# Performance work log

Measured on AMD Instinct MI355X. Metric: run time of the kernel, lower is better.

## Reference

```python
import jax, jax.numpy as jnp
import numpy as np

N, B, D = 2048, 2, 512
H, R = 8, 3
C = D // H  # head dim = 64


def setup_inputs() -> dict:
    key = jax.random.key(0)
    ks = jax.random.split(key, 12)
    x_q = jax.random.normal(ks[0], (N, B, D), jnp.float32)
    x_k = jax.random.normal(ks[1], (N, B, D), jnp.float32)
    x_v = jax.random.normal(ks[2], (N, B, D), jnp.float32)
    attn_mask = jax.random.randint(ks[3], (B, R, N, N), 0, 2).astype(bool)
    # pad the last 128 key positions (realistic padding; avoids all -inf rows)
    key_padding_mask = jnp.zeros((B, N), bool).at[:, -128:].set(True)
    s = 1.0 / np.sqrt(D)
    Wq = jax.random.normal(ks[4], (D, D), jnp.float32) * s
    Wk = jax.random.normal(ks[5], (D, D), jnp.float32) * s
    Wv = jax.random.normal(ks[6], (D, D), jnp.float32) * s
    Wo = jax.random.normal(ks[7], (D, D), jnp.float32) * s
    bq = jnp.zeros((D,), jnp.float32)
    bk = jnp.zeros((D,), jnp.float32)
    bv = jnp.zeros((D,), jnp.float32)
    bo = jnp.zeros((D,), jnp.float32)
    # mask_weight: randn, last column set to sqrt(head_dim) as in __init__
    mask_weight = jax.random.normal(ks[8], (H, R + 1), jnp.float32)
    mask_weight = mask_weight.at[:, -1].set(np.sqrt(C))
    return dict(x_q=x_q, x_k=x_k, x_v=x_v, attn_mask=attn_mask,
                key_padding_mask=key_padding_mask, Wq=Wq, bq=bq, Wk=Wk, bk=bk,
                Wv=Wv, bv=bv, Wo=Wo, bo=bo, mask_weight=mask_weight)


def _split_heads(x):
    # (n, b, h*c) -> (b, h, n, c)
    n, b, _ = x.shape
    return jnp.transpose(x.reshape(n, b, H, C), (1, 2, 0, 3))


def reference(x_q, x_k, x_v, attn_mask, key_padding_mask,
              Wq, bq, Wk, bk, Wv, bv, Wo, bo, mask_weight):
    q = _split_heads(x_q @ Wq + bq)  # (b,h,n,c)
    k = _split_heads(x_k @ Wk + bk)
    v = _split_heads(x_v @ Wv + bv)

    # relative bias: softmax over edge-type weights, scaled per head
    rel_w = jax.nn.softmax(mask_weight[:, :-1], axis=-1)  # (h,r)
    inv_mask = (~attn_mask).astype(jnp.float32)           # (b,r,n,m)
    rel = jnp.einsum('hr,h,brnm->bhnm', rel_w, mask_weight[:, -1], inv_mask)
    rel = jnp.where(key_padding_mask[:, None, None, :], -jnp.inf, rel)

    # scaled dot-product attention (torch default scale = 1/sqrt(head_dim))
    scores = jnp.einsum('bhnc,bhmc->bhnm', q, k) * (1.0 / np.sqrt(C))
    attn = jax.nn.softmax(scores + rel, axis=-1)
    o = jnp.einsum('bhnm,bhmc->bhnc', attn, v)

    # (b,h,n,c) -> (n,b,h*c)
    n = o.shape[2]
    o = jnp.transpose(o, (2, 0, 1, 3)).reshape(n, o.shape[0], H * C)
    return o @ Wo + bo
```

## Files before the change

### kernel.cpp

```cpp
#include <hip/hip_runtime.h>
#include <hip/hip_bf16.h>

#define NN 2048
#define LOG2E 1.4426950408889634f

typedef unsigned int u32;
typedef unsigned short u16;
typedef unsigned char u8;

typedef __attribute__((ext_vector_type(8))) short short8;
typedef __attribute__((ext_vector_type(4))) float f32x4;

__device__ __forceinline__ u16 f2bf(float f){
  __hip_bfloat16 h = __float2bfloat16(f);
  return *reinterpret_cast<u16*>(&h);
}
__device__ __forceinline__ u32 pack2(float a, float b){
  return (u32)f2bf(a) | ((u32)f2bf(b) << 16);
}
__device__ __forceinline__ void gload16(const void* g, void* l){
  __builtin_amdgcn_global_load_lds((const __attribute__((address_space(1))) u32*)g,
                                   (__attribute__((address_space(3))) u32*)l, 16, 0, 0);
}

__global__ __launch_bounds__(256)
void prep_k(const int* __restrict__ am, const int* __restrict__ kp,
            u8* __restrict__ cmb)
{
  const size_t tid  = (size_t)blockIdx.x * 256 + threadIdx.x;
  const size_t base = tid * 4;
  const int row = (int)(base >> 11);
  const int m0  = (int)(base & 2047);
  const int b = row >> 11, n = row & 2047;
  const size_t e0 = (((size_t)(b*3) * NN) + n) * NN + m0;
  const int4 a0 = *reinterpret_cast<const int4*>(am + e0);
  const int4 a1 = *reinterpret_cast<const int4*>(am + e0 + (size_t)NN*NN);
  const int4 a2 = *reinterpret_cast<const int4*>(am + e0 + 2*(size_t)NN*NN);
  const int4 kv = *reinterpret_cast<const int4*>(kp + (size_t)b*NN + m0);
  const int a0v[4] = {a0.x,a0.y,a0.z,a0.w};
  const int a1v[4] = {a1.x,a1.y,a1.z,a1.w};
  const int a2v[4] = {a2.x,a2.y,a2.z,a2.w};
  const int kvv[4] = {kv.x,kv.y,kv.z,kv.w};
  uchar4 out;
  u8* o = (u8*)&out;
  #pragma unroll
  for (int i = 0; i < 4; ++i)
    o[i] = (u8)((a0v[i]?1:0) | (a1v[i]?2:0) | (a2v[i]?4:0) | (kvv[i]?8:0));
  *reinterpret_cast<uchar4*>(cmb + base) = out;
}

__global__ __launch_bounds__(256)
void trw3_k(const float* __restrict__ W0, const float* __restrict__ W1,
            const float* __restrict__ W2, u16* __restrict__ WT)
{
  __shared__ float tile[32][33];
  const float* W = (blockIdx.z == 0) ? W0 : (blockIdx.z == 1) ? W1 : W2;
  u16* dst = WT + (size_t)blockIdx.z * 262144;
  const int t = threadIdx.x;
  const int k0 = blockIdx.x * 32, n0 = blockIdx.y * 32;
  const int c = t & 31, r = t >> 5;
  #pragma unroll
  for (int i = 0; i < 4; ++i)
    tile[r + 8*i][c] = W[(size_t)(k0 + r + 8*i) * 512 + n0 + c];
  __syncthreads();
  #pragma unroll
  for (int i = 0; i < 4; ++i)
    dst[(size_t)(n0 + r + 8*i) * 512 + k0 + c] = f2bf(tile[c][r + 8*i]);
}

__global__ __launch_bounds__(256)
void trw_k(const float* __restrict__ W, u16* __restrict__ WT)
{
  __shared__ float tile[32][33];
  const int t = threadIdx.x;
  const int k0 = blockIdx.x * 32, n0 = blockIdx.y * 32;
  const int c = t & 31, r = t >> 5;
  #pragma unroll
  for (int i = 0; i < 4; ++i)
    tile[r + 8*i][c] = W[(size_t)(k0 + r + 8*i) * 512 + n0 + c];
  __syncthreads();
  #pragma unroll
  for (int i = 0; i < 4; ++i)
    WT[(size_t)(n0 + r + 8*i) * 512 + k0 + c] = f2bf(tile[c][r + 8*i]);
}

template<int BN, bool SCATTER, bool ABF16, bool OUTF32>
__device__ __forceinline__
void gemm_core(const void* __restrict__ Av, const u16* __restrict__ WT,
               const float* __restrict__ bias, void* __restrict__ Cd,
               float scale, int m0, int n0)
{
  constexpr int NI  = BN / 64;
  constexpr int WNL = BN / 32;
  __shared__ u16 As[2][64*64];
  __shared__ u16 Ws[2][BN*64];

  const int t = threadIdx.x;
  const int lane = t & 63;
  const int w = t >> 6;
  const int g = lane >> 4, r15 = lane & 15;
  const int wn = w * (BN/4);

  const int arow = t >> 2, akc = (t & 3) * 16, as0 = (t & 3) * 2;
  const int wrn = (BN==128) ? (t>>1) : (t>>2);
  const int wkc = (BN==128) ? ((t&1)*32) : ((t&3)*16);
  const int wsb = (BN==128) ? ((t&1)*4)  : ((t&3)*2);

  uint4  war[WNL];
  uint4  aab[2];
  float4 aaf[4];

  auto loadA = [&](int k0){
    if constexpr (ABF16) {
      const u16* A = (const u16*)Av;
      aab[0] = *reinterpret_cast<const uint4*>(A + (size_t)(m0+arow)*512 + k0 + akc);
      aab[1] = *reinterpret_cast<const uint4*>(A + (size_t)(m0+arow)*512 + k0 + akc + 8);
    } else {
      const float* A = (const float*)Av;
      #pragma unroll
      for (int q = 0; q < 4; ++q)
        aaf[q] = *reinterpret_cast<const float4*>(A + (size_t)(m0+arow)*512 + k0 + akc + 4*q);
    }
  };
  auto loadW = [&](int k0){
    #pragma unroll
    for (int i = 0; i < WNL; ++i)
      war[i] = *reinterpret_cast<const uint4*>(WT + (size_t)(n0+wrn)*512 + k0 + wkc + 8*i);
  };
  auto writeA = [&](int bf){
    uint4 v0, v1;
    if constexpr (ABF16) { v0 = aab[0]; v1 = aab[1]; }
    else {
      v0.x = pack2(aaf[0].x, aaf[0].y); v0.y = pack2(aaf[0].z, aaf[0].w);
      v0.z = pack2(aaf[1].x, aaf[1].y); v0.w = pack2(aaf[1].z, aaf[1].w);
      v1.x = pack2(aaf[2].x, aaf[2].y); v1.y = pack2(aaf[2].z, aaf[2].w);
      v1.z = pack2(aaf[3].x, aaf[3].y); v1.w = pack2(aaf[3].z, aaf[3].w);
    }
    *reinterpret_cast<uint4*>(&As[bf][arow*64 + (((as0  ) ^ (arow&7)) << 3)]) = v0;
    *reinterpret_cast<uint4*>(&As[bf][arow*64 + (((as0+1) ^ (arow&7)) << 3)]) = v1;
  };
  auto writeW = [&](int bf){
    #pragma unroll
    for (int i = 0; i < WNL; ++i)
      *reinterpret_cast<uint4*>(&Ws[bf][wrn*64 + (((wsb+i) ^ (wrn&7)) << 3)]) = war[i];
  };

  const f32x4 fz = {0.f,0.f,0.f,0.f};
  f32x4 acc[4][NI];
  #pragma unroll
  for (int mi = 0; mi < 4; ++mi)
    #pragma unroll
    for (int ni = 0; ni < NI; ++ni) acc[mi][ni] = fz;

  loadA(0); loadW(0);
  writeA(0); writeW(0);
  __syncthreads();

  for (int kt = 0; kt < 8; ++kt) {
    const int cur = kt & 1;
    if (kt < 7) { loadA((kt+1)*64); loadW((kt+1)*64); }
    #pragma unroll
    for (int ks = 0; ks < 2; ++ks) {
      short8 bfr[NI], afr[4];
      #pragma unroll
      for (int ni = 0; ni < NI; ++ni) {
        const int n = wn + 16*ni + r15;
        bfr[ni] = *reinterpret_cast<const short8*>(&Ws[cur][n*64 + (((ks*4+g) ^ (n&7)) << 3)]);
      }
      #pragma unroll
      for (int mi = 0; mi < 4; ++mi) {
        const int m = 16*mi + r15;
        afr[mi] = *reinterpret_cast<const short8*>(&As[cur][m*64 + (((ks*4+g) ^ (m&7)) << 3)]);
      }
      #pragma unroll
      for (int mi = 0; mi < 4; ++mi)
        #pragma unroll
        for (int ni = 0; ni < NI; ++ni)
          acc[mi][ni] = __builtin_amdgcn_mfma_f32_16x16x32_bf16(afr[mi], bfr[ni], acc[mi][ni], 0, 0, 0);
    }
    if (kt < 7) { writeA(cur^1); writeW(cur^1); }
    __syncthreads();
  }

  float bia[NI];
  #pragma unroll
  for (int ni = 0; ni < NI; ++ni) bia[ni] = bias[n0 + wn + 16*ni + r15];
  #pragma unroll
  for (int mi = 0; mi < 4; ++mi) {
    #pragma unroll
    for (int ni = 0; ni < NI; ++ni) {
      #pragma unroll
      for (int j = 0; j < 4; ++j) {
        const int row = m0 + 16*mi + 4*g + j;
        const int col = n0 + wn + 16*ni + r15;
        const float v = (acc[mi][ni][j] + bia[ni]) * scale;
        if constexpr (SCATTER) {
          const int bb = row & 1, ntok = row >> 1;
          const int h = col >> 6, c = col & 63;
          ((u16*)Cd)[(((size_t)(bb*8 + h) * NN + ntok) * 64) + c] = f2bf(v);
        } else if constexpr (OUTF32) {
          ((float*)Cd)[(size_t)row * 512 + col] = v;
        } else {
          ((u16*)Cd)[(size_t)row * 512 + col] = f2bf(v);
        }
      }
    }
  }
}

__global__ __launch_bounds__(256)
void gemm_qkv(const float* __restrict__ x0, const float* __restrict__ x1,
              const float* __restrict__ x2, const u16* __restrict__ WT3,
              const float* __restrict__ b0, const float* __restrict__ b1,
              const float* __restrict__ b2, u16* __restrict__ dst, float qscale)
{
  const int z = blockIdx.z;
  const float* A    = (z == 0) ? x0 : (z == 1) ? x1 : x2;
  const float* bias = (z == 0) ? b0 : (z == 1) ? b1 : b2;
  gemm_core<128, true, false, false>(A, WT3 + (size_t)z*262144, bias,
                                     dst + (size_t)z*2097152,
                                     (z == 0) ? qscale : 1.0f,
                                     blockIdx.x*64, blockIdx.y*128);
}

__global__ __launch_bounds__(256)
void gemm_wo(const u16* __restrict__ Ob, const u16* __restrict__ WT,
             const float* __restrict__ bias, float* __restrict__ out)
{
  gemm_core<64, false, true, true>(Ob, WT, bias, out, 1.0f,
                                   blockIdx.x*64, blockIdx.y*64);
}

__global__ __launch_bounds__(512)
void attn_mfma(const u16* __restrict__ Q, const u16* __restrict__ K,
               const u16* __restrict__ V, const u8* __restrict__ cmb,
               const float* __restrict__ mw, u16* __restrict__ O,
               float* __restrict__ Opart, float2* __restrict__ Ml, int kspan)
{
  __shared__ u16 Ks[2][64*64];
  __shared__ u16 Vs[2][64*64];
  __shared__ float lut[16];

  const int t = threadIdx.x;
  const int lane = t & 63;
  const int w = t >> 6;
  const int g = lane >> 4;
  const int r15 = lane & 15;
  const int bh = blockIdx.y;
  const int z = blockIdx.z;
  const int b = bh >> 3, h = bh & 7;
  const int n0 = blockIdx.x * 128;
  const int nq = n0 + w*16 + r15;
  const int k_beg = z * kspan;
  const float NEGINF = -__builtin_inff();

  if (t < 16) {
    const float mw0 = mw[h*4+0], mw1 = mw[h*4+1], mw2 = mw[h*4+2];
    const float msc = mw[h*4+3];
    const float mxw = fmaxf(mw0, fmaxf(mw1, mw2));
    const float e0 = __expf(mw0-mxw), e1 = __expf(mw1-mxw), e2 = __expf(mw2-mxw);
    const float inv = msc / (e0+e1+e2);
    float v = ((t & 1) ? 0.f : e0*inv) + ((t & 2) ? 0.f : e1*inv)
            + ((t & 4) ? 0.f : e2*inv);
    lut[t] = (t & 8) ? NEGINF : v * LOG2E;
  }

  const u16* qrow = Q + ((size_t)bh*NN + nq)*64;
  const short8 bq0 = *reinterpret_cast<const short8*>(qrow + 8*g);
  const short8 bq1 = *reinterpret_cast<const short8*>(qrow + 32 + 8*g);

  const u8* crow = cmb + ((size_t)(b*NN + nq))*NN;
  const u16* Kbase = K + (size_t)bh*NN*64;
  const u16* Vbase = V + (size_t)bh*NN*64;

  float m_run = NEGINF, l_run = 0.f;
  const f32x4 fz = {0.f, 0.f, 0.f, 0.f};
  f32x4 oacc[4] = {fz, fz, fz, fz};

  const int sm  = t >> 3;
  const int ssl = t & 7;
  const int kcol = (ssl ^ (sm & 7)) * 8;
  const int sc0 = (t & 7) * 8;
  const int aA = (((g & 1) << 5) + r15) << 2;
  const int aB = aA + 64;

  uint4 vreg;
  auto gloadK = [&](int m0, int bf){
    gload16(Kbase + (size_t)(m0 + sm)*64 + kcol, &Ks[bf][w*512 + (lane << 3)]);
  };
  auto loadV = [&](int m0){
    vreg = *reinterpret_cast<const uint4*>(Vbase + (size_t)(m0 + sm)*64 + sc0);
  };
  auto writeV = [&](int bf){
    u16 e[8];
    e[0]=vreg.x&0xffff; e[1]=vreg.x>>16; e[2]=vreg.y&0xffff; e[3]=vreg.y>>16;
    e[4]=vreg.z&0xffff; e[5]=vreg.z>>16; e[6]=vreg.w&0xffff; e[7]=vreg.w>>16;
    #pragma unroll
    for (int i = 0; i < 8; ++i) {
      const int c = sc0 + i;
      Vs[bf][c*64 + ((((sm>>3) ^ (c&7) ^ (c>>3)) << 3) | (sm & 7))] = e[i];
    }
  };

  const int ntiles = kspan >> 6;
  gloadK(k_beg, 0);
  loadV(k_beg);
  writeV(0);
  __syncthreads();

  for (int it = 0; it < ntiles; ++it) {
    const int cur = it & 1;
    const int m0 = k_beg + it * 64;
    const bool more = (it + 1 < ntiles);
    if (more) { gloadK(m0 + 64, cur ^ 1); loadV(m0 + 64); }

    float sv[4][4];
    #pragma unroll
    for (int kt = 0; kt < 4; ++kt) {
      const int key = 16*kt + r15;
      const short8 a0 = *reinterpret_cast<const short8*>(&Ks[cur][key*64 + (((g  ) ^ (key&7)) << 3)]);
      const short8 a1 = *reinterpret_cast<const short8*>(&Ks[cur][key*64 + (((g+4) ^ (key&7)) << 3)]);
      f32x4 s = fz;
      s = __builtin_amdgcn_mfma_f32_16x16x32_bf16(a0, bq0, s, 0, 0, 0);
      s = __builtin_amdgcn_mfma_f32_16x16x32_bf16(a1, bq1, s, 0, 0, 0);
      const u32 cw = *reinterpret_cast<const u32*>(crow + m0 + 16*kt + 4*g);
      #pragma unroll
      for (int j = 0; j < 4; ++j)
        sv[kt][j] = s[j] + lut[(cw >> (8*j)) & 0xfu];
    }
    float pmax = NEGINF;
    #pragma unroll
    for (int kt = 0; kt < 4; ++kt)
      #pragma unroll
      for (int j = 0; j < 4; ++j) pmax = fmaxf(pmax, sv[kt][j]);
    float tmax = pmax;
    tmax = fmaxf(tmax, __shfl_xor(tmax, 16));
    tmax = fmaxf(tmax, __shfl_xor(tmax, 32));

    const bool skip = __all((m_run != NEGINF) && (tmax <= m_run + 10.0f));
    float nm = m_run, sc = 1.0f;
    if (!skip) {
      nm = fmaxf(m_run, tmax);
      if (nm != NEGINF) { sc = exp2f(m_run - nm); m_run = nm; }
      #pragma unroll
      for (int ct = 0; ct < 4; ++ct) oacc[ct] *= sc;
    }

    float psum = 0.f;
    const bool hig = (g >= 2);

    {
      u32 wp[2][2];
      #pragma unroll
      for (int kt = 0; kt < 2; ++kt) {
        float p[4];
        #pragma unroll
        for (int j = 0; j < 4; ++j) {
          p[j] = (nm == NEGINF) ? 0.f : exp2f(sv[kt][j] - nm);
          psum += p[j];
        }
        wp[kt][0] = pack2(p[0], p[1]);
        wp[kt][1] = pack2(p[2], p[3]);
      }
      const u32 e0 = __builtin_amdgcn_ds_bpermute(aA, (int)wp[0][0]);
      const u32 e1 = __builtin_amdgcn_ds_bpermute(aA, (int)wp[0][1]);
      const u32 e2 = __builtin_amdgcn_ds_bpermute(aB, (int)wp[0][0]);
      const u32 e3 = __builtin_amdgcn_ds_bpermute(aB, (int)wp[0][1]);
      const u32 f0 = __builtin_amdgcn_ds_bpermute(aA, (int)wp[1][0]);
      const u32 f1 = __builtin_amdgcn_ds_bpermute(aA, (int)wp[1][1]);
      const u32 f2 = __builtin_amdgcn_ds_bpermute(aB, (int)wp[1][0]);
      const u32 f3 = __builtin_amdgcn_ds_bpermute(aB, (int)wp[1][1]);
      union { uint4 u; short8 s; } cv;
      cv.u = make_uint4(hig ? f0 : e0, hig ? f1 : e1, hig ? f2 : e2, hig ? f3 : e3);
      const short8 bp0 = cv.s;
      #pragma unroll
      for (int ct = 0; ct < 4; ++ct) {
        const int c = 16*ct + r15;
        const short8 av0 = *reinterpret_cast<const short8*>(
          &Vs[cur][c*64 + ((((g  ) ^ (c&7) ^ (c>>3))) << 3)]);
        oacc[ct] = __builtin_amdgcn_mfma_f32_16x16x32_bf16(av0, bp0, oacc[ct], 0, 0, 0);
      }
    }
    {
      u32 wp[2][2];
      #pragma unroll
      for (int kt = 0; kt < 2; ++kt) {
        float p[4];
        #pragma unroll
        for (int j = 0; j < 4; ++j) {
          p[j] = (nm == NEGINF) ? 0.f : exp2f(sv[kt+2][j] - nm);
          psum += p[j];
        }
        wp[kt][0] = pack2(p[0], p[1]);
        wp[kt][1] = pack2(p[2], p[3]);
      }
      const u32 e0 = __builtin_amdgcn_ds_bpermute(aA, (int)wp[0][0]);
      const u32 e1 = __builtin_amdgcn_ds_bpermute(aA, (int)wp[0][1]);
      const u32 e2 = __builtin_amdgcn_ds_bpermute(aB, (int)wp[0][0]);
      const u32 e3 = __builtin_amdgcn_ds_bpermute(aB, (int)wp[0][1]);
      const u32 f0 = __builtin_amdgcn_ds_bpermute(aA, (int)wp[1][0]);
      const u32 f1 = __builtin_amdgcn_ds_bpermute(aA, (int)wp[1][1]);
      const u32 f2 = __builtin_amdgcn_ds_bpermute(aB, (int)wp[1][0]);
      const u32 f3 = __builtin_amdgcn_ds_bpermute(aB, (int)wp[1][1]);
      union { uint4 u; short8 s; } cv;
      cv.u = make_uint4(hig ? f0 : e0, hig ? f1 : e1, hig ? f2 : e2, hig ? f3 : e3);
      const short8 bp1 = cv.s;
      #pragma unroll
      for (int ct = 0; ct < 4; ++ct) {
        const int c = 16*ct + r15;
        const short8 av1 = *reinterpret_cast<const short8*>(
          &Vs[cur][c*64 + ((((g+4) ^ (c&7) ^ (c>>3))) << 3)]);
        oacc[ct] = __builtin_amdgcn_mfma_f32_16x16x32_bf16(av1, bp1, oacc[ct], 0, 0, 0);
      }
    }

    psum += __shfl_xor(psum, 16);
    psum += __shfl_xor(psum, 32);
    l_run = l_run * sc + psum;

    if (more) writeV(cur ^ 1);
    __syncthreads();
  }

  if (Opart) {
    float* orow = Opart + (((size_t)(z*16 + bh)) * NN + nq) * 64;
    #pragma unroll
    for (int ct = 0; ct < 4; ++ct)
      *reinterpret_cast<float4*>(orow + 16*ct + 4*g) =
        make_float4(oacc[ct][0], oacc[ct][1], oacc[ct][2], oacc[ct][3]);
    if (g == 0)
      Ml[((size_t)(z*16 + bh)) * NN + nq] = make_float2(m_run, l_run);
  } else {
    const float rinv = 1.f / l_run;
    #pragma unroll
    for (int ct = 0; ct < 4; ++ct) {
      u16* dst = O + ((size_t)(nq*2 + b))*512 + h*64 + 16*ct + 4*g;
      *reinterpret_cast<ushort4*>(dst) =
        make_ushort4(f2bf(oacc[ct][0]*rinv), f2bf(oacc[ct][1]*rinv),
                     f2bf(oacc[ct][2]*rinv), f2bf(oacc[ct][3]*rinv));
    }
  }
}

__global__ __launch_bounds__(256)
void combine_k(const float* __restrict__ Opart, const float2* __restrict__ Ml,
               u16* __restrict__ Ob, int nsplit)
{
  const int t = threadIdx.x;
  const int lane = t & 63, w = t >> 6;
  const int q = blockIdx.x * 4 + w;
  const int bh = blockIdx.y;
  const int b = bh >> 3, h = bh & 7;

  float M = -__builtin_inff();
  for (int s = 0; s < nsplit; ++s)
    M = fmaxf(M, Ml[((size_t)(s*16 + bh)) * NN + q].x);

  float num = 0.f, den = 0.f;
  for (int s = 0; s < nsplit; ++s) {
    const float2 ml = Ml[((size_t)(s*16 + bh)) * NN + q];
    const float ws = (ml.x == -__builtin_inff()) ? 0.f : exp2f(ml.x - M);
    den += ws * ml.y;
    num += ws * Opart[(((size_t)(s*16 + bh)) * NN + q) * 64 + lane];
  }
  const float r = (den > 0.f) ? num / den : 0.f;
  Ob[((size_t)(q*2 + b)) * 512 + h*64 + lane] = f2bf(r);
}

extern "C" void kernel_launch(void* const* d_in, const int* in_sizes, int n_in,
                              void* d_out, int out_size, void* d_ws, size_t ws_size,
                              hipStream_t stream)
{
  const float* xq = (const float*)d_in[0];
  const float* xk = (const float*)d_in[1];
  const float* xv = (const float*)d_in[2];
  const int*   am = (const int*)d_in[3];
  const int*   kp = (const int*)d_in[4];
  const float* Wq = (const float*)d_in[5];
  const float* bq = (const float*)d_in[6];
  const float* Wk = (const float*)d_in[7];
  const float* bk = (const float*)d_in[8];
  const float* Wv = (const float*)d_in[9];
  const float* bv = (const float*)d_in[10];
  const float* Wo = (const float*)d_in[11];
  const float* bo = (const float*)d_in[12];
  const float* mw = (const float*)d_in[13];

  u16* Qb = (u16*)d_ws;
  u16* Kb = Qb + (size_t)16*NN*64;
  u16* Vb = Kb + (size_t)16*NN*64;
  u16* Ob = Vb + (size_t)16*NN*64;
  u8*  cmb = (u8*)(Ob + (size_t)4096*512);
  u8*  R   = cmb + (size_t)2*NN*NN;

  u16*   WT3   = (u16*)R;
  float* Opart = (float*)R;
  const size_t base_bytes = (size_t)(R - (u8*)d_ws);
  int nsplit = 1;
  for (int s = 4; s >= 1; s >>= 1) {
    const size_t need = base_bytes + (size_t)s * 16 * NN * (64*4 + 8);
    if (need <= ws_size) { nsplit = s; break; }
  }
  float2* Ml = (float2*)(Opart + (size_t)nsplit * 16 * NN * 64);
  const bool split = (base_bytes + (size_t)16*NN*(64*4+8) <= ws_size) &&
                     (base_bytes + (size_t)3*512*512*2 <= ws_size);
  u16* WTo = Qb;

  prep_k<<<(2*NN*NN/4 + 255)/256, 256, 0, stream>>>(am, kp, cmb);

  const float qscale = 0.125f * LOG2E;
  trw3_k<<<dim3(16, 16, 3), 256, 0, stream>>>(Wq, Wk, Wv, WT3);
  gemm_qkv<<<dim3(64, 4, 3), 256, 0, stream>>>(xq, xk, xv, WT3, bq, bk, bv, Qb, qscale);

  if (split) {
    attn_mfma<<<dim3(16, 16, nsplit), 512, 0, stream>>>(Qb, Kb, Vb, cmb, mw, Ob,
                                                        Opart, Ml, NN / nsplit);
    combine_k<<<dim3(NN/4, 16), 256, 0, stream>>>(Opart, Ml, Ob, nsplit);
  } else {
    attn_mfma<<<dim3(16, 16, 1), 512, 0, stream>>>(Qb, Kb, Vb, cmb, mw, Ob,
                                                   nullptr, nullptr, NN);
  }
  trw_k<<<dim3(16, 16), 256, 0, stream>>>(Wo, WTo);
  gemm_wo<<<dim3(64, 8), 256, 0, stream>>>(Ob, WTo, bo, (float*)d_out);
}
```

Measured before the change: 130.2 us.

## Process two query sub-tiles per wave to reuse K/V LDS fragments

The attention kernel now runs 4 waves of 256 threads instead of 8. Each wave handles 32 query rows as two 16-row sub-tiles, so every K and V fragment read from LDS feeds two MFMAs. Each thread loads twice as many K/V rows per tile. This halves LDS read traffic per query and the cost of staging K/V. In exchange, register pressure roughly doubles for the accumulators and scores, and there are fewer waves per block to hide latency.

```diff
diff --git a/kernel.cpp b/kernel.cpp
--- a/kernel.cpp
+++ b/kernel.cpp
@@ -231,7 +231,7 @@
                                    blockIdx.x*64, blockIdx.y*64);
 }
 
-__global__ __launch_bounds__(512)
+__global__ __launch_bounds__(256)
 void attn_mfma(const u16* __restrict__ Q, const u16* __restrict__ K,
                const u16* __restrict__ V, const u8* __restrict__ cmb,
                const float* __restrict__ mw, u16* __restrict__ O,
@@ -250,7 +250,6 @@
   const int z = blockIdx.z;
   const int b = bh >> 3, h = bh & 7;
   const int n0 = blockIdx.x * 128;
-  const int nq = n0 + w*16 + r15;
   const int k_beg = z * kspan;
   const float NEGINF = -__builtin_inff();
 
@@ -265,40 +264,54 @@
     lut[t] = (t & 8) ? NEGINF : v * LOG2E;
   }
 
-  const u16* qrow = Q + ((size_t)bh*NN + nq)*64;
-  const short8 bq0 = *reinterpret_cast<const short8*>(qrow + 8*g);
-  const short8 bq1 = *reinterpret_cast<const short8*>(qrow + 32 + 8*g);
-
-  const u8* crow = cmb + ((size_t)(b*NN + nq))*NN;
+  const int nqb = n0 + w*32 + r15;
+  short8 bq[2][2];
+  #pragma unroll
+  for (int qa = 0; qa < 2; ++qa) {
+    const u16* qrow = Q + ((size_t)bh*NN + nqb + 16*qa)*64;
+    bq[qa][0] = *reinterpret_cast<const short8*>(qrow + 8*g);
+    bq[qa][1] = *reinterpret_cast<const short8*>(qrow + 32 + 8*g);
+  }
+  const u8* crow[2] = { cmb + ((size_t)(b*NN + nqb))*NN,
+                        cmb + ((size_t)(b*NN + nqb + 16))*NN };
+
   const u16* Kbase = K + (size_t)bh*NN*64;
   const u16* Vbase = V + (size_t)bh*NN*64;
 
-  float m_run = NEGINF, l_run = 0.f;
+  float m_run[2] = {NEGINF, NEGINF}, l_run[2] = {0.f, 0.f};
   const f32x4 fz = {0.f, 0.f, 0.f, 0.f};
-  f32x4 oacc[4] = {fz, fz, fz, fz};
-
-  const int sm  = t >> 3;
-  const int ssl = t & 7;
-  const int kcol = (ssl ^ (sm & 7)) * 8;
-  const int sc0 = (t & 7) * 8;
+  f32x4 oacc[2][4] = {{fz,fz,fz,fz},{fz,fz,fz,fz}};
+
+  const int r0 = t >> 3;
+  const int sl = t & 7;
+  const int kcol = (sl ^ (r0 & 7)) * 8;
+  const int sc0v = sl * 8;
   const int aA = (((g & 1) << 5) + r15) << 2;
   const int aB = aA + 64;
-
-  uint4 vreg;
+  const bool hig = (g >= 2);
+
+  uint4 vreg0, vreg1;
   auto gloadK = [&](int m0, int bf){
-    gload16(Kbase + (size_t)(m0 + sm)*64 + kcol, &Ks[bf][w*512 + (lane << 3)]);
+    gload16(Kbase + (size_t)(m0 + r0)*64 + kcol,      &Ks[bf][t << 3]);
+    gload16(Kbase + (size_t)(m0 + r0 + 32)*64 + kcol, &Ks[bf][(t << 3) + 2048]);
   };
   auto loadV = [&](int m0){
-    vreg = *reinterpret_cast<const uint4*>(Vbase + (size_t)(m0 + sm)*64 + sc0);
+    vreg0 = *reinterpret_cast<const uint4*>(Vbase + (size_t)(m0 + r0)*64 + sc0v);
+    vreg1 = *reinterpret_cast<const uint4*>(Vbase + (size_t)(m0 + r0 + 32)*64 + sc0v);
   };
   auto writeV = [&](int bf){
-    u16 e[8];
-    e[0]=vreg.x&0xffff; e[1]=vreg.x>>16; e[2]=vreg.y&0xffff; e[3]=vreg.y>>16;
-    e[4]=vreg.z&0xffff; e[5]=vreg.z>>16; e[6]=vreg.w&0xffff; e[7]=vreg.w>>16;
-    #pragma unroll
-    for (int i = 0; i < 8; ++i) {
-      const int c = sc0 + i;
-      Vs[bf][c*64 + ((((sm>>3) ^ (c&7) ^ (c>>3)) << 3) | (sm & 7))] = e[i];
+    #pragma unroll
+    for (int half = 0; half < 2; ++half) {
+      const uint4 vv = half ? vreg1 : vreg0;
+      const int r = r0 + 32*half;
+      u16 e[8];
+      e[0]=vv.x&0xffff; e[1]=vv.x>>16; e[2]=vv.y&0xffff; e[3]=vv.y>>16;
+      e[4]=vv.z&0xffff; e[5]=vv.z>>16; e[6]=vv.w&0xffff; e[7]=vv.w>>16;
+      #pragma unroll
+      for (int i = 0; i < 8; ++i) {
+        const int c = sc0v + i;
+        Vs[bf][c*64 + ((((r>>3) ^ (c&7) ^ (c>>3)) << 3) | (r & 7))] = e[i];
+      }
     }
   };
 
@@ -314,130 +327,116 @@
     const bool more = (it + 1 < ntiles);
     if (more) { gloadK(m0 + 64, cur ^ 1); loadV(m0 + 64); }
 
-    float sv[4][4];
+    float sv[2][4][4];
     #pragma unroll
     for (int kt = 0; kt < 4; ++kt) {
       const int key = 16*kt + r15;
       const short8 a0 = *reinterpret_cast<const short8*>(&Ks[cur][key*64 + (((g  ) ^ (key&7)) << 3)]);
       const short8 a1 = *reinterpret_cast<const short8*>(&Ks[cur][key*64 + (((g+4) ^ (key&7)) << 3)]);
-      f32x4 s = fz;
-      s = __builtin_amdgcn_mfma_f32_16x16x32_bf16(a0, bq0, s, 0, 0, 0);
-      s = __builtin_amdgcn_mfma_f32_16x16x32_bf16(a1, bq1, s, 0, 0, 0);
-      const u32 cw = *reinterpret_cast<const u32*>(crow + m0 + 16*kt + 4*g);
-      #pragma unroll
-      for (int j = 0; j < 4; ++j)
-        sv[kt][j] = s[j] + lut[(cw >> (8*j)) & 0xfu];
-    }
-    float pmax = NEGINF;
-    #pragma unroll
-    for (int kt = 0; kt < 4; ++kt)
-      #pragma unroll
-      for (int j = 0; j < 4; ++j) pmax = fmaxf(pmax, sv[kt][j]);
-    float tmax = pmax;
-    tmax = fmaxf(tmax, __shfl_xor(tmax, 16));
-    tmax = fmaxf(tmax, __shfl_xor(tmax, 32));
-
-    const bool skip = __all((m_run != NEGINF) && (tmax <= m_run + 10.0f));
-    float nm = m_run, sc = 1.0f;
-    if (!skip) {
-      nm = fmaxf(m_run, tmax);
-      if (nm != NEGINF) { sc = exp2f(m_run - nm); m_run = nm; }
-      #pragma unroll
-      for (int ct = 0; ct < 4; ++ct) oacc[ct] *= sc;
-    }
-
-    float psum = 0.f;
-    const bool hig = (g >= 2);
-
-    {
-      u32 wp[2][2];
-      #pragma unroll
-      for (int kt = 0; kt < 2; ++kt) {
-        float p[4];
+      #pragma unroll
+      for (int qa = 0; qa < 2; ++qa) {
+        f32x4 s = fz;
+        s = __builtin_amdgcn_mfma_f32_16x16x32_bf16(a0, bq[qa][0], s, 0, 0, 0);
+        s = __builtin_amdgcn_mfma_f32_16x16x32_bf16(a1, bq[qa][1], s, 0, 0, 0);
+        const u32 cw = *reinterpret_cast<const u32*>(crow[qa] + m0 + 16*kt + 4*g);
         #pragma unroll
-        for (int j = 0; j < 4; ++j) {
-          p[j] = (nm == NEGINF) ? 0.f : exp2f(sv[kt][j] - nm);
-          psum += p[j];
+        for (int j = 0; j < 4; ++j)
+          sv[qa][kt][j] = s[j] + lut[(cw >> (8*j)) & 0xfu];
+      }
+    }
+
+    float nm[2], sc[2];
+    #pragma unroll
+    for (int qa = 0; qa < 2; ++qa) {
+      float pmax = NEGINF;
+      #pragma unroll
+      for (int kt = 0; kt < 4; ++kt)
+        #pragma unroll
+        for (int j = 0; j < 4; ++j) pmax = fmaxf(pmax, sv[qa][kt][j]);
+      float tmax = pmax;
+      tmax = fmaxf(tmax, __shfl_xor(tmax, 16));
+      tmax = fmaxf(tmax, __shfl_xor(tmax, 32));
+      const bool skip = __all((m_run[qa] != NEGINF) && (tmax <= m_run[qa] + 10.0f));
+      nm[qa] = m_run[qa]; sc[qa] = 1.0f;
+      if (!skip) {
+        nm[qa] = fmaxf(m_run[qa], tmax);
+        if (nm[qa] != NEGINF) { sc[qa] = exp2f(m_run[qa] - nm[qa]); m_run[qa] = nm[qa]; }
+        #pragma unroll
+        for (int ct = 0; ct < 4; ++ct) oacc[qa][ct] *= sc[qa];
+      }
+    }
+
+    float psum[2] = {0.f, 0.f};
+    #pragma unroll
+    for (int half = 0; half < 2; ++half) {
+      short8 bp[2];
+      #pragma unroll
+      for (int qa = 0; qa < 2; ++qa) {
+        u32 wp[2][2];
+        #pragma unroll
+        for (int kt = 0; kt < 2; ++kt) {
+          float p[4];
+          #pragma unroll
+          for (int j = 0; j < 4; ++j) {
+            p[j] = (nm[qa] == NEGINF) ? 0.f : exp2f(sv[qa][2*half + kt][j] - nm[qa]);
+            psum[qa] += p[j];
+          }
+          wp[kt][0] = pack2(p[0], p[1]);
+          wp[kt][1] = pack2(p[2], p[3]);
         }
-        wp[kt][0] = pack2(p[0], p[1]);
-        wp[kt][1] = pack2(p[2], p[3]);
-      }
-      const u32 e0 = __builtin_amdgcn_ds_bpermute(aA, (int)wp[0][0]);
-      const u32 e1 = __builtin_amdgcn_ds_bpermute(aA, (int)wp[0][1]);
-      const u32 e2 = __builtin_amdgcn_ds_bpermute(aB, (int)wp[0][0]);
-      const u32 e3 = __builtin_amdgcn_ds_bpermute(aB, (int)wp[0][1]);
-      const u32 f0 = __builtin_amdgcn_ds_bpermute(aA, (int)wp[1][0]);
-      const u32 f1 = __builtin_amdgcn_ds_bpermute(aA, (int)wp[1][1]);
-      const u32 f2 = __builtin_amdgcn_ds_bpermute(aB, (int)wp[1][0]);
-      const u32 f3 = __builtin_amdgcn_ds_bpermute(aB, (int)wp[1][1]);
-      union { uint4 u; short8 s; } cv;
-      cv.u = make_uint4(hig ? f0 : e0, hig ? f1 : e1, hig ? f2 : e2, hig ? f3 : e3);
-      const short8 bp0 = cv.s;
+        const u32 e0 = __builtin_amdgcn_ds_bpermute(aA, (int)wp[0][0]);
+        const u32 e1 = __builtin_amdgcn_ds_bpermute(aA, (int)wp[0][1]);
+        const u32 e2 = __builtin_amdgcn_ds_bpermute(aB, (int)wp[0][0]);
+        const u32 e3 = __builtin_amdgcn_ds_bpermute(aB, (int)wp[0][1]);
+        const u32 f0 = __builtin_amdgcn_ds_bpermute(aA, (int)wp[1][0]);
+        const u32 f1 = __builtin_amdgcn_ds_bpermute(aA, (int)wp[1][1]);
+        const u32 f2 = __builtin_amdgcn_ds_bpermute(aB, (int)wp[1][0]);
+        const u32 f3 = __builtin_amdgcn_ds_bpermute(aB, (int)wp[1][1]);
+        union { uint4 u; short8 s; } cv;
+        cv.u = make_uint4(hig ? f0 : e0, hig ? f1 : e1, hig ? f2 : e2, hig ? f3 : e3);
+        bp[qa] = cv.s;
+      }
       #pragma unroll
       for (int ct = 0; ct < 4; ++ct) {
         const int c = 16*ct + r15;
-        const short8 av0 = *reinterpret_cast<const short8*>(
-          &Vs[cur][c*64 + ((((g  ) ^ (c&7) ^ (c>>3))) << 3)]);
-        oacc[ct] = __builtin_amdgcn_mfma_f32_16x16x32_bf16(av0, bp0, oacc[ct], 0, 0, 0);
-      }
-    }
-    {
-      u32 wp[2][2];
-      #pragma unroll
-      for (int kt = 0; kt < 2; ++kt) {
-        float p[4];
-        #pragma unroll
-        for (int j = 0; j < 4; ++j) {
-          p[j] = (nm == NEGINF) ? 0.f : exp2f(sv[kt+2][j] - nm);
-          psum += p[j];
-        }
-        wp[kt][0] = pack2(p[0], p[1]);
-        wp[kt][1] = pack2(p[2], p[3]);
-      }
-      const u32 e0 = __builtin_amdgcn_ds_bpermute(aA, (int)wp[0][0]);
-      const u32 e1 = __builtin_amdgcn_ds_bpermute(aA, (int)wp[0][1]);
-      const u32 e2 = __builtin_amdgcn_ds_bpermute(aB, (int)wp[0][0]);
-      const u32 e3 = __builtin_amdgcn_ds_bpermute(aB, (int)wp[0][1]);
-      const u32 f0 = __builtin_amdgcn_ds_bpermute(aA, (int)wp[1][0]);
-      const u32 f1 = __builtin_amdgcn_ds_bpermute(aA, (int)wp[1][1]);
-      const u32 f2 = __builtin_amdgcn_ds_bpermute(aB, (int)wp[1][0]);
-      const u32 f3 = __builtin_amdgcn_ds_bpermute(aB, (int)wp[1][1]);
-      union { uint4 u; short8 s; } cv;
-      cv.u = make_uint4(hig ? f0 : e0, hig ? f1 : e1, hig ? f2 : e2, hig ? f3 : e3);
-      const short8 bp1 = cv.s;
-      #pragma unroll
-      for (int ct = 0; ct < 4; ++ct) {
-        const int c = 16*ct + r15;
-        const short8 av1 = *reinterpret_cast<const short8*>(
-          &Vs[cur][c*64 + ((((g+4) ^ (c&7) ^ (c>>3))) << 3)]);
-        oacc[ct] = __builtin_amdgcn_mfma_f32_16x16x32_bf16(av1, bp1, oacc[ct], 0, 0, 0);
-      }
-    }
-
-    psum += __shfl_xor(psum, 16);
-    psum += __shfl_xor(psum, 32);
-    l_run = l_run * sc + psum;
+        const int slot = (half ? (g+4) : g) ^ (c&7) ^ (c>>3);
+        const short8 av = *reinterpret_cast<const short8*>(&Vs[cur][c*64 + (slot << 3)]);
+        oacc[0][ct] = __builtin_amdgcn_mfma_f32_16x16x32_bf16(av, bp[0], oacc[0][ct], 0, 0, 0);
+        oacc[1][ct] = __builtin_amdgcn_mfma_f32_16x16x32_bf16(av, bp[1], oacc[1][ct], 0, 0, 0);
+      }
+    }
+
+    #pragma unroll
+    for (int qa = 0; qa < 2; ++qa) {
+      psum[qa] += __shfl_xor(psum[qa], 16);
+      psum[qa] += __shfl_xor(psum[qa], 32);
+      l_run[qa] = l_run[qa] * sc[qa] + psum[qa];
+    }
 
     if (more) writeV(cur ^ 1);
     __syncthreads();
   }
 
-  if (Opart) {
-    float* orow = Opart + (((size_t)(z*16 + bh)) * NN + nq) * 64;
-    #pragma unroll
-    for (int ct = 0; ct < 4; ++ct)
-      *reinterpret_cast<float4*>(orow + 16*ct + 4*g) =
-        make_float4(oacc[ct][0], oacc[ct][1], oacc[ct][2], oacc[ct][3]);
-    if (g == 0)
-      Ml[((size_t)(z*16 + bh)) * NN + nq] = make_float2(m_run, l_run);
-  } else {
-    const float rinv = 1.f / l_run;
-    #pragma unroll
-    for (int ct = 0; ct < 4; ++ct) {
-      u16* dst = O + ((size_t)(nq*2 + b))*512 + h*64 + 16*ct + 4*g;
-      *reinterpret_cast<ushort4*>(dst) =
-        make_ushort4(f2bf(oacc[ct][0]*rinv), f2bf(oacc[ct][1]*rinv),
-                     f2bf(oacc[ct][2]*rinv), f2bf(oacc[ct][3]*rinv));
+  #pragma unroll
+  for (int qa = 0; qa < 2; ++qa) {
+    const int nq = nqb + 16*qa;
+    if (Opart) {
+      float* orow = Opart + (((size_t)(z*16 + bh)) * NN + nq) * 64;
+      #pragma unroll
+      for (int ct = 0; ct < 4; ++ct)
+        *reinterpret_cast<float4*>(orow + 16*ct + 4*g) =
+          make_float4(oacc[qa][ct][0], oacc[qa][ct][1], oacc[qa][ct][2], oacc[qa][ct][3]);
+      if (g == 0)
+        Ml[((size_t)(z*16 + bh)) * NN + nq] = make_float2(m_run[qa], l_run[qa]);
+    } else {
+      const float rinv = 1.f / l_run[qa];
+      #pragma unroll
+      for (int ct = 0; ct < 4; ++ct) {
+        u16* dst = O + ((size_t)(nq*2 + b))*512 + h*64 + 16*ct + 4*g;
+        *reinterpret_cast<ushort4*>(dst) =
+          make_ushort4(f2bf(oacc[qa][ct][0]*rinv), f2bf(oacc[qa][ct][1]*rinv),
+                       f2bf(oacc[qa][ct][2]*rinv), f2bf(oacc[qa][ct][3]*rinv));
+      }
     }
   }
 }
@@ -513,11 +512,11 @@
   gemm_qkv<<<dim3(64, 4, 3), 256, 0, stream>>>(xq, xk, xv, WT3, bq, bk, bv, Qb, qscale);
 
   if (split) {
-    attn_mfma<<<dim3(16, 16, nsplit), 512, 0, stream>>>(Qb, Kb, Vb, cmb, mw, Ob,
+    attn_mfma<<<dim3(16, 16, nsplit), 256, 0, stream>>>(Qb, Kb, Vb, cmb, mw, Ob,
                                                         Opart, Ml, NN / nsplit);
     combine_k<<<dim3(NN/4, 16), 256, 0, stream>>>(Opart, Ml, Ob, nsplit);
   } else {
-    attn_mfma<<<dim3(16, 16, 1), 512, 0, stream>>>(Qb, Kb, Vb, cmb, mw, Ob,
+    attn_mfma<<<dim3(16, 16, 1), 256, 0, stream>>>(Qb, Kb, Vb, cmb, mw, Ob,
                                                    nullptr, nullptr, NN);
   }
   trw_k<<<dim3(16, 16), 256, 0, stream>>>(Wo, WTo);
```

Result: slower. 137.7 us (+5.8%).

## Stage softmax probabilities through LDS and store split partials in bf16

Applied to the files above, without the earlier changes.

Replaces the ds_bpermute shuffles that rearranged P into MFMA B-operand layout with a per-wave swizzled LDS staging buffer. Each lane writes its P fragment and reads back two short8 operands, so all eight MFMAs issue in one block. Separately, split-K partial outputs are stored as bf16 instead of fp32, halving Opart traffic in attention and combine. This also lets larger nsplit fit in the workspace. The costs are extra LDS use and stores, and lower precision of the unnormalized partial accumulators.

```diff
diff --git a/kernel.cpp b/kernel.cpp
--- a/kernel.cpp
+++ b/kernel.cpp
@@ -15,6 +15,7 @@
   __hip_bfloat16 h = __float2bfloat16(f);
   return *reinterpret_cast<u16*>(&h);
 }
+__device__ __forceinline__ float bf1(u16 u){ return __uint_as_float(((u32)u) << 16); }
 __device__ __forceinline__ u32 pack2(float a, float b){
   return (u32)f2bf(a) | ((u32)f2bf(b) << 16);
 }
@@ -235,10 +236,11 @@
 void attn_mfma(const u16* __restrict__ Q, const u16* __restrict__ K,
                const u16* __restrict__ V, const u8* __restrict__ cmb,
                const float* __restrict__ mw, u16* __restrict__ O,
-               float* __restrict__ Opart, float2* __restrict__ Ml, int kspan)
+               u16* __restrict__ Opart, float2* __restrict__ Ml, int kspan)
 {
   __shared__ u16 Ks[2][64*64];
   __shared__ u16 Vs[2][64*64];
+  __shared__ u16 Ps[8][16*64];
   __shared__ float lut[16];
 
   const int t = threadIdx.x;
@@ -281,8 +283,6 @@
   const int ssl = t & 7;
   const int kcol = (ssl ^ (sm & 7)) * 8;
   const int sc0 = (t & 7) * 8;
-  const int aA = (((g & 1) << 5) + r15) << 2;
-  const int aB = aA + 64;
 
   uint4 vreg;
   auto gloadK = [&](int m0, int bf){
@@ -347,87 +347,47 @@
     }
 
     float psum = 0.f;
-    const bool hig = (g >= 2);
-
-    {
-      u32 wp[2][2];
-      #pragma unroll
-      for (int kt = 0; kt < 2; ++kt) {
-        float p[4];
-        #pragma unroll
-        for (int j = 0; j < 4; ++j) {
-          p[j] = (nm == NEGINF) ? 0.f : exp2f(sv[kt][j] - nm);
-          psum += p[j];
-        }
-        wp[kt][0] = pack2(p[0], p[1]);
-        wp[kt][1] = pack2(p[2], p[3]);
+    #pragma unroll
+    for (int kt = 0; kt < 4; ++kt) {
+      float p[4];
+      #pragma unroll
+      for (int j = 0; j < 4; ++j) {
+        p[j] = (nm == NEGINF) ? 0.f : exp2f(sv[kt][j] - nm);
+        psum += p[j];
       }
-      const u32 e0 = __builtin_amdgcn_ds_bpermute(aA, (int)wp[0][0]);
-      const u32 e1 = __builtin_amdgcn_ds_bpermute(aA, (int)wp[0][1]);
-      const u32 e2 = __builtin_amdgcn_ds_bpermute(aB, (int)wp[0][0]);
-      const u32 e3 = __builtin_amdgcn_ds_bpermute(aB, (int)wp[0][1]);
-      const u32 f0 = __builtin_amdgcn_ds_bpermute(aA, (int)wp[1][0]);
-      const u32 f1 = __builtin_amdgcn_ds_bpermute(aA, (int)wp[1][1]);
-      const u32 f2 = __builtin_amdgcn_ds_bpermute(aB, (int)wp[1][0]);
-      const u32 f3 = __builtin_amdgcn_ds_bpermute(aB, (int)wp[1][1]);
-      union { uint4 u; short8 s; } cv;
-      cv.u = make_uint4(hig ? f0 : e0, hig ? f1 : e1, hig ? f2 : e2, hig ? f3 : e3);
-      const short8 bp0 = cv.s;
-      #pragma unroll
-      for (int ct = 0; ct < 4; ++ct) {
-        const int c = 16*ct + r15;
-        const short8 av0 = *reinterpret_cast<const short8*>(
-          &Vs[cur][c*64 + ((((g  ) ^ (c&7) ^ (c>>3))) << 3)]);
-        oacc[ct] = __builtin_amdgcn_mfma_f32_16x16x32_bf16(av0, bp0, oacc[ct], 0, 0, 0);
-      }
-    }
-    {
-      u32 wp[2][2];
-      #pragma unroll
-      for (int kt = 0; kt < 2; ++kt) {
-        float p[4];
-        #pragma unroll
-        for (int j = 0; j < 4; ++j) {
-          p[j] = (nm == NEGINF) ? 0.f : exp2f(sv[kt+2][j] - nm);
-          psum += p[j];
-        }
-        wp[kt][0] = pack2(p[0], p[1]);
-        wp[kt][1] = pack2(p[2], p[3]);
-      }
-      const u32 e0 = __builtin_amdgcn_ds_bpermute(aA, (int)wp[0][0]);
-      const u32 e1 = __builtin_amdgcn_ds_bpermute(aA, (int)wp[0][1]);
-      const u32 e2 = __builtin_amdgcn_ds_bpermute(aB, (int)wp[0][0]);
-      const u32 e3 = __builtin_amdgcn_ds_bpermute(aB, (int)wp[0][1]);
-      const u32 f0 = __builtin_amdgcn_ds_bpermute(aA, (int)wp[1][0]);
-      const u32 f1 = __builtin_amdgcn_ds_bpermute(aA, (int)wp[1][1]);
-      const u32 f2 = __builtin_amdgcn_ds_bpermute(aB, (int)wp[1][0]);
-      const u32 f3 = __builtin_amdgcn_ds_bpermute(aB, (int)wp[1][1]);
-      union { uint4 u; short8 s; } cv;
-      cv.u = make_uint4(hig ? f0 : e0, hig ? f1 : e1, hig ? f2 : e2, hig ? f3 : e3);
-      const short8 bp1 = cv.s;
-      #pragma unroll
-      for (int ct = 0; ct < 4; ++ct) {
-        const int c = 16*ct + r15;
-        const short8 av1 = *reinterpret_cast<const short8*>(
-          &Vs[cur][c*64 + ((((g+4) ^ (c&7) ^ (c>>3))) << 3)]);
-        oacc[ct] = __builtin_amdgcn_mfma_f32_16x16x32_bf16(av1, bp1, oacc[ct], 0, 0, 0);
-      }
-    }
-
+      const int slot = 2*kt + (g >> 1);
+      const int off  = 4 * (g & 1);
+      *reinterpret_cast<ushort4*>(&Ps[w][r15*64 + ((slot ^ (r15 & 7)) << 3) + off]) =
+        make_ushort4(f2bf(p[0]), f2bf(p[1]), f2bf(p[2]), f2bf(p[3]));
+    }
     psum += __shfl_xor(psum, 16);
     psum += __shfl_xor(psum, 32);
     l_run = l_run * sc + psum;
 
+    const short8 bp0 = *reinterpret_cast<const short8*>(&Ps[w][r15*64 + (((g  ) ^ (r15 & 7)) << 3)]);
+    const short8 bp1 = *reinterpret_cast<const short8*>(&Ps[w][r15*64 + (((g+4) ^ (r15 & 7)) << 3)]);
+    #pragma unroll
+    for (int ct = 0; ct < 4; ++ct) {
+      const int c = 16*ct + r15;
+      const short8 av0 = *reinterpret_cast<const short8*>(
+        &Vs[cur][c*64 + ((((g  ) ^ (c&7) ^ (c>>3))) << 3)]);
+      const short8 av1 = *reinterpret_cast<const short8*>(
+        &Vs[cur][c*64 + ((((g+4) ^ (c&7) ^ (c>>3))) << 3)]);
+      oacc[ct] = __builtin_amdgcn_mfma_f32_16x16x32_bf16(av0, bp0, oacc[ct], 0, 0, 0);
+      oacc[ct] = __builtin_amdgcn_mfma_f32_16x16x32_bf16(av1, bp1, oacc[ct], 0, 0, 0);
+    }
+
     if (more) writeV(cur ^ 1);
     __syncthreads();
   }
 
   if (Opart) {
-    float* orow = Opart + (((size_t)(z*16 + bh)) * NN + nq) * 64;
+    u16* orow = Opart + (((size_t)(z*16 + bh)) * NN + nq) * 64;
     #pragma unroll
     for (int ct = 0; ct < 4; ++ct)
-      *reinterpret_cast<float4*>(orow + 16*ct + 4*g) =
-        make_float4(oacc[ct][0], oacc[ct][1], oacc[ct][2], oacc[ct][3]);
+      *reinterpret_cast<ushort4*>(orow + 16*ct + 4*g) =
+        make_ushort4(f2bf(oacc[ct][0]), f2bf(oacc[ct][1]),
+                     f2bf(oacc[ct][2]), f2bf(oacc[ct][3]));
     if (g == 0)
       Ml[((size_t)(z*16 + bh)) * NN + nq] = make_float2(m_run, l_run);
   } else {
@@ -443,7 +403,7 @@
 }
 
 __global__ __launch_bounds__(256)
-void combine_k(const float* __restrict__ Opart, const float2* __restrict__ Ml,
+void combine_k(const u16* __restrict__ Opart, const float2* __restrict__ Ml,
                u16* __restrict__ Ob, int nsplit)
 {
   const int t = threadIdx.x;
@@ -461,7 +421,7 @@
     const float2 ml = Ml[((size_t)(s*16 + bh)) * NN + q];
     const float ws = (ml.x == -__builtin_inff()) ? 0.f : exp2f(ml.x - M);
     den += ws * ml.y;
-    num += ws * Opart[(((size_t)(s*16 + bh)) * NN + q) * 64 + lane];
+    num += ws * bf1(Opart[(((size_t)(s*16 + bh)) * NN + q) * 64 + lane]);
   }
   const float r = (den > 0.f) ? num / den : 0.f;
   Ob[((size_t)(q*2 + b)) * 512 + h*64 + lane] = f2bf(r);
@@ -493,16 +453,16 @@
   u8*  cmb = (u8*)(Ob + (size_t)4096*512);
   u8*  R   = cmb + (size_t)2*NN*NN;
 
-  u16*   WT3   = (u16*)R;
-  float* Opart = (float*)R;
+  u16* WT3   = (u16*)R;
+  u16* Opart = (u16*)R;
   const size_t base_bytes = (size_t)(R - (u8*)d_ws);
   int nsplit = 1;
   for (int s = 4; s >= 1; s >>= 1) {
-    const size_t need = base_bytes + (size_t)s * 16 * NN * (64*4 + 8);
+    const size_t need = base_bytes + (size_t)s * 16 * NN * (64*2 + 8);
     if (need <= ws_size) { nsplit = s; break; }
   }
   float2* Ml = (float2*)(Opart + (size_t)nsplit * 16 * NN * 64);
-  const bool split = (base_bytes + (size_t)16*NN*(64*4+8) <= ws_size) &&
+  const bool split = (base_bytes + (size_t)16*NN*(64*2+8) <= ws_size) &&
                      (base_bytes + (size_t)3*512*512*2 <= ws_size);
   u16* WTo = Qb;
 
```

Result: faster. 122.9 us (-5.6%).
